# Optimization experiments

Measured on AMD Instinct MI355X. Metric: run time of the kernel, lower is better.

Reference implementation:

```python
import jax, jax.numpy as jnp
import numpy as np

B, H, V, L, M, D, C = 64, 512, 50000, 400, 128, 64, 64
HC = 2 * D + M + 4  # controller LSTM hidden size (one head)
EPS = 1e-8


def _lstm_step(x, h, c, Wih, Whh, bih, bhh):
    g = x @ Wih.T + bih + h @ Whh.T + bhh
    i, f, gg, o = jnp.split(g, 4, axis=-1)
    c2 = jax.nn.sigmoid(f) * c + jax.nn.sigmoid(i) * jnp.tanh(gg)
    return jax.nn.sigmoid(o) * jnp.tanh(c2), c2


def _head_params(hc):
    # slices exactly as in LSTMMemoryController (k=0, single head)
    keys = hc[:, :M]                               # [B, M]
    kstr = jnp.exp(hc[:, D:D + 1])                 # [B, 1]
    gate = jax.nn.sigmoid(hc[:, D + 1:D + 2])      # [B, 1]
    erase = jax.nn.sigmoid(hc[:, D + 4:M + D + 4]) # [B, M]
    add = jax.nn.sigmoid(hc[:, 2 * D + 4:M + 2 * D + 4])  # [B, M]
    return keys, kstr, gate, erase, add


def _addressing(keys, kstr, gate, heads, memory):
    # torch cosine_similarity(keys.unsqueeze(2), memory, dim=2):
    # keys [B,M] broadcast along memory_dim D
    num = keys * memory.sum(-1)                                   # [B, M]
    nk = jnp.maximum(jnp.abs(keys) * jnp.sqrt(jnp.float32(D)), EPS)
    nm = jnp.maximum(jnp.linalg.norm(memory, axis=-1), EPS)
    cos = num / (nk * nm)
    content = jax.nn.softmax(kstr * cos, axis=1)                  # [B, M]
    # faithful to original: heads[k] indexes axis 0 (k=0) -> shape [1, M]
    gated = gate * content + (1.0 - gate) * heads[0]
    return gated[:, None, :]                                      # [B, 1, M]


def reference(input_ids, h0, c0, encoder_outputs, word_occurrence_indicator,
              coverage, memory, read_heads, write_heads,
              read_h, read_c, write_h, write_c,
              emb, attn_W, attn_b, cov_W, state_W, comb_W, comb_b,
              rpre_W, rpre_b, wpre_W, wpre_b,
              r_Wih, r_Whh, r_bih, r_bhh,
              w_Wih, w_Whh, w_bih, w_bhh,
              l_Wih, l_Whh, l_bih, l_bhh,
              out_W, out_b):
    embedded = emb[input_ids]                                     # [B, H]
    ia = jnp.concatenate([embedded, h0], 1) @ attn_W.T + attn_b  # [B, L]
    tc = (coverage + ia) @ cov_W.T
    ts = c0 @ state_W.T
    aw = jax.nn.softmax(tc + ia + ts, axis=1)                     # [B, L]
    attn_applied = jnp.einsum('bl,blh->bh', aw, encoder_outputs)  # [B, H]
    out0 = jnp.concatenate([embedded, attn_applied], 1) @ comb_W.T + comb_b  # [B, H]

    hm = jnp.concatenate([h0, memory.reshape(-1, M * D)], 1)
    rh, rc = _lstm_step(hm @ rpre_W.T + rpre_b, read_h, read_c, r_Wih, r_Whh, r_bih, r_bhh)
    wh, wc = _lstm_step(hm @ wpre_W.T + wpre_b, write_h, write_c, w_Wih, w_Whh, w_bih, w_bhh)
    rk, rks, rg, _, _ = _head_params(rh)
    wk, wks, wg, we, wa = _head_params(wh)
    rw = _addressing(rk, rks, rg, read_heads, memory)             # [B, 1, M]
    ww = _addressing(wk, wks, wg, write_heads, memory)            # [B, 1, M]

    read_in = jnp.einsum('bkm,bmd->bkd', rw, memory).reshape(-1, D)
    h1, c1 = _lstm_step(jnp.concatenate([out0, read_in], 1), h0, c0,
                        l_Wih, l_Whh, l_bih, l_bhh)
    # residual (h1 + out0) is computed in the original but unused by its output path

    w0 = ww[:, 0, :, None]                                        # [B, M, 1]
    new_memory = memory * (1.0 - w0 * we[:, :, None]) + w0 * wa[:, :, None]
    new_coverage = coverage + ia

    log_probs = jax.nn.log_softmax(c1[:, None, :] @ out_W.T + out_b, axis=-1)  # [B, 1, V]
    return log_probs, h1, c1, new_memory, new_coverage


def setup_inputs() -> dict:
    key = jax.random.key(0)
    ks = iter(jax.random.split(key, 48))

    def rn(shape, fan_in):
        return jax.random.normal(next(ks), shape, jnp.float32) / np.sqrt(fan_in)

    inp = {
        'input_ids': jax.random.randint(next(ks), (B,), 0, V),
        'h0': jax.random.normal(next(ks), (B, H), jnp.float32),
        'c0': jax.random.normal(next(ks), (B, H), jnp.float32),
        'encoder_outputs': jax.random.normal(next(ks), (B, L, H), jnp.float32),
        'word_occurrence_indicator': jnp.zeros((B, L), jnp.float32),
        'coverage': jnp.zeros((B, L), jnp.float32),
        'memory': jax.random.normal(next(ks), (B, M, D), jnp.float32),
        'read_heads': jnp.zeros((B, 1, M), jnp.float32),
        'write_heads': jnp.zeros((B, 1, M), jnp.float32),
        'read_h': jnp.zeros((B, HC), jnp.float32),
        'read_c': jnp.zeros((B, HC), jnp.float32),
        'write_h': jnp.zeros((B, HC), jnp.float32),
        'write_c': jnp.zeros((B, HC), jnp.float32),
        'emb': rn((V, H), H),
        'attn_W': rn((L, 2 * H), 2 * H), 'attn_b': jnp.zeros((L,), jnp.float32),
        'cov_W': rn((L, L), L),
        'state_W': rn((L, H), H),
        'comb_W': rn((H, 2 * H), 2 * H), 'comb_b': jnp.zeros((H,), jnp.float32),
        'rpre_W': rn((C, M * D + H), M * D + H), 'rpre_b': jnp.zeros((C,), jnp.float32),
        'wpre_W': rn((C, M * D + H), M * D + H), 'wpre_b': jnp.zeros((C,), jnp.float32),
        'r_Wih': rn((4 * HC, C), C), 'r_Whh': rn((4 * HC, HC), HC),
        'r_bih': jnp.zeros((4 * HC,), jnp.float32), 'r_bhh': jnp.zeros((4 * HC,), jnp.float32),
        'w_Wih': rn((4 * HC, C), C), 'w_Whh': rn((4 * HC, HC), HC),
        'w_bih': jnp.zeros((4 * HC,), jnp.float32), 'w_bhh': jnp.zeros((4 * HC,), jnp.float32),
        'l_Wih': rn((4 * H, H + D), H + D), 'l_Whh': rn((4 * H, H), H),
        'l_bih': jnp.zeros((4 * H,), jnp.float32), 'l_bhh': jnp.zeros((4 * H,), jnp.float32),
        'out_W': rn((V, H), H), 'out_b': jnp.zeros((V,), jnp.float32),
    }
    return inp
```

## Files before the change

### kernel.cpp

```cpp
#include <hip/hip_runtime.h>
#include <math.h>

#define BB 64
#define HH 512
#define VV 50000
#define LL 400
#define MM 128
#define DD 64
#define HC 260
#define EPSF 1e-8f

typedef __attribute__((ext_vector_type(8))) short bf16x8;
typedef __attribute__((ext_vector_type(4))) float f32x4;
typedef __attribute__((address_space(1))) const void CGV;
typedef __attribute__((address_space(3))) void LV;

__device__ __forceinline__ float sigmoidf(float x){ return 1.0f/(1.0f+expf(-x)); }
__device__ __forceinline__ unsigned short bf16_rne(float f){
  unsigned u = __float_as_uint(f);
  return (unsigned short)((u + 0x7fffu + ((u >> 16) & 1u)) >> 16);
}
__device__ __forceinline__ float wave_max(float v){
  #pragma unroll
  for(int o=32;o;o>>=1) v = fmaxf(v, __shfl_xor(v,o));
  return v;
}
__device__ __forceinline__ float wave_sum(float v){
  #pragma unroll
  for(int o=32;o;o>>=1) v += __shfl_xor(v,o);
  return v;
}
__device__ __forceinline__ float dot4(float4 a, float4 w){
  return a.x*w.x + a.y*w.y + a.z*w.z + a.w*w.w;
}

__global__ __launch_bounds__(256) void k_ia_ts(const int* __restrict__ ids,
    const float* __restrict__ emb, const float* __restrict__ h0,
    const float* __restrict__ c0, const float* __restrict__ attn_W,
    const float* __restrict__ attn_b, const float* __restrict__ state_W,
    float* __restrict__ ia, float* __restrict__ ts){
  int b = blockIdx.y;
  int wid = threadIdx.x >> 6, lane = threadIdx.x & 63;
  if (blockIdx.x < 100){
    int n = blockIdx.x*4 + wid;
    const float4* E4 = (const float4*)(emb + (long)ids[b]*HH);
    const float4* H4 = (const float4*)(h0 + (long)b*HH);
    const float4* W4 = (const float4*)(attn_W + (long)n*1024);
    float acc = 0.f;
    #pragma unroll
    for (int i = 0; i < 4; i++){
      int k = lane + i*64;
      float4 a = (k < 128) ? E4[k] : H4[k-128];
      acc += dot4(a, W4[k]);
    }
    acc = wave_sum(acc);
    if (lane == 0) ia[b*LL + n] = acc + attn_b[n];
  } else {
    int n = (blockIdx.x-100)*4 + wid;
    const float4* A4 = (const float4*)(c0 + (long)b*HH);
    const float4* W4 = (const float4*)(state_W + (long)n*HH);
    float acc = 0.f;
    #pragma unroll
    for (int i = 0; i < 2; i++){
      int k = lane + i*64;
      acc += dot4(A4[k], W4[k]);
    }
    acc = wave_sum(acc);
    if (lane == 0) ts[b*LL + n] = acc;
  }
}

__global__ __launch_bounds__(256) void k_tc_cov(const float* __restrict__ cov,
    const float* __restrict__ ia, const float* __restrict__ cov_W,
    float* __restrict__ tc, float* __restrict__ ncov){
  int b = blockIdx.y;
  int wid = threadIdx.x >> 6, lane = threadIdx.x & 63;
  int n = blockIdx.x*4 + wid;
  const float4* C4 = (const float4*)(cov + (long)b*LL);
  const float4* I4 = (const float4*)(ia + (long)b*LL);
  const float4* W4 = (const float4*)(cov_W + (long)n*LL);
  float acc = 0.f;
  #pragma unroll
  for (int i = 0; i < 2; i++){
    int k = lane + i*64;
    if (k < 100){
      float4 a = C4[k], a2 = I4[k], w = W4[k];
      acc += (a.x+a2.x)*w.x + (a.y+a2.y)*w.y + (a.z+a2.z)*w.z + (a.w+a2.w)*w.w;
    }
  }
  acc = wave_sum(acc);
  if (lane == 0){
    tc[b*LL + n] = acc;
    ncov[b*LL + n] = cov[b*LL + n] + ia[b*LL + n];
  }
}

__global__ __launch_bounds__(256) void k_attn_part(const float* __restrict__ ia,
                                                   const float* __restrict__ ts,
                                                   const float* __restrict__ tc,
                                                   const float* __restrict__ enc,
                                                   float* __restrict__ part){
  int b = blockIdx.x, lc = blockIdx.y, t = threadIdx.x;
  __shared__ float sh[400];
  __shared__ float sm[4], ss[4];
  int i0 = t, i1 = t + 256;
  float x0 = ia[b*LL+i0] + ts[b*LL+i0] + tc[b*LL+i0];
  float x1 = (i1 < LL) ? (ia[b*LL+i1] + ts[b*LL+i1] + tc[b*LL+i1]) : -INFINITY;
  float m = wave_max(fmaxf(x0, x1));
  if ((t & 63) == 0) sm[t>>6] = m;
  __syncthreads();
  m = fmaxf(fmaxf(sm[0], sm[1]), fmaxf(sm[2], sm[3]));
  float e0 = expf(x0 - m);
  float e1 = (i1 < LL) ? expf(x1 - m) : 0.0f;
  sh[i0] = e0;
  if (i1 < LL) sh[i1] = e1;
  float s = wave_sum(e0 + e1);
  if ((t & 63) == 0) ss[t>>6] = s;
  __syncthreads();
  float inv = 1.0f / (ss[0] + ss[1] + ss[2] + ss[3]);
  const float* eb = enc + ((long)b*LL + lc*25)*HH;
  float a0 = 0.f, a1 = 0.f;
  for (int l = 0; l < 25; l++){
    float a = sh[lc*25 + l] * inv;
    a0 += a * eb[(long)l*HH + t];
    a1 += a * eb[(long)l*HH + t + 256];
  }
  part[((b*16 + lc) << 9) + t]       = a0;
  part[((b*16 + lc) << 9) + t + 256] = a1;
}

__global__ void k_attn_reduce(const float* __restrict__ part, float* __restrict__ attn){
  int idx = blockIdx.x*256 + threadIdx.x;
  if (idx >= BB*HH) return;
  int b = idx >> 9, h = idx & 511;
  float s = 0.f;
  #pragma unroll
  for (int lc = 0; lc < 16; lc++) s += part[((b*16 + lc) << 9) + h];
  attn[b*HH + h] = s;
}

__global__ __launch_bounds__(256) void k_comb(const int* __restrict__ ids,
    const float* __restrict__ emb, const float* __restrict__ attn,
    const float* __restrict__ comb_W, const float* __restrict__ comb_b,
    float* __restrict__ xcat3){
  int b = blockIdx.y;
  int wid = threadIdx.x >> 6, lane = threadIdx.x & 63;
  int n = blockIdx.x*4 + wid;
  const float4* E4 = (const float4*)(emb + (long)ids[b]*HH);
  const float4* A4 = (const float4*)(attn + (long)b*HH);
  const float4* W4 = (const float4*)(comb_W + (long)n*1024);
  float acc = 0.f;
  #pragma unroll
  for (int i = 0; i < 4; i++){
    int k = lane + i*64;
    float4 a = (k < 128) ? E4[k] : A4[k-128];
    acc += dot4(a, W4[k]);
  }
  acc = wave_sum(acc);
  if (lane == 0) xcat3[b*576 + n] = acc + comb_b[n];
}

__global__ __launch_bounds__(256) void k_pre(const float* __restrict__ h0,
    const float* __restrict__ mem, const float* __restrict__ rW,
    const float* __restrict__ wW, const float* __restrict__ rb,
    const float* __restrict__ wb, float* __restrict__ pre_r,
    float* __restrict__ pre_w){
  int wid = threadIdx.x >> 6, lane = threadIdx.x & 63;
  int n = blockIdx.x*4 + wid;
  int b = blockIdx.y;
  int which = blockIdx.z;
  const float* W = which ? wW : rW;
  const float4* W4 = (const float4*)(W + (long)n*8704);
  const float4* H4 = (const float4*)(h0 + (long)b*HH);
  const float4* M4 = (const float4*)(mem + (long)b*8192);
  float acc = 0.f;
  #pragma unroll 4
  for (int i = 0; i < 34; i++){
    int k = lane + i*64;
    float4 a = (k < 128) ? H4[k] : M4[k-128];
    acc += dot4(a, W4[k]);
  }
  acc = wave_sum(acc);
  if (lane == 0) (which ? pre_w : pre_r)[b*64 + n] = acc + (which ? wb : rb)[n];
}

__global__ __launch_bounds__(256) void k_gates(const float* __restrict__ pre_r,
    const float* __restrict__ pre_w, const float* __restrict__ read_h,
    const float* __restrict__ write_h, const float* __restrict__ read_c,
    const float* __restrict__ write_c,
    const float* __restrict__ rWih, const float* __restrict__ rWhh,
    const float* __restrict__ rbih, const float* __restrict__ rbhh,
    const float* __restrict__ wWih, const float* __restrict__ wWhh,
    const float* __restrict__ wbih, const float* __restrict__ wbhh,
    float* __restrict__ rh, float* __restrict__ wh){
  int which = blockIdx.z, b = blockIdx.y;
  int wid = threadIdx.x >> 6, lane = threadIdx.x & 63;
  int j = blockIdx.x*4 + wid;
  const float* pre = which ? pre_w : pre_r;
  const float* hhv = which ? write_h : read_h;
  const float* Wih = which ? wWih : rWih;
  const float* Whh = which ? wWhh : rWhh;
  float pv = pre[b*64 + lane];
  const float* hb = hhv + b*HC;
  float gv[4];
  #pragma unroll
  for (int g = 0; g < 4; g++){
    int n = g*HC + j;
    float acc = pv * Wih[n*64 + lane];
    const float* wr = Whh + (long)n*HC;
    #pragma unroll
    for (int i = 0; i < 5; i++){
      int k = lane + i*64;
      if (k < HC) acc += hb[k]*wr[k];
    }
    gv[g] = wave_sum(acc);
  }
  if (lane == 0){
    #pragma unroll
    for (int g = 0; g < 4; g++) gv[g] += (which ? wbih : rbih)[g*HC+j] + (which ? wbhh : rbhh)[g*HC+j];
    float c2 = sigmoidf(gv[1]) * (which ? write_c : read_c)[b*HC + j]
             + sigmoidf(gv[0]) * tanhf(gv[2]);
    (which ? wh : rh)[b*HC + j] = sigmoidf(gv[3]) * tanhf(c2);
  }
}

__global__ __launch_bounds__(128) void k_addr_mem(const float* __restrict__ rh,
                                                  const float* __restrict__ whv,
                                                  const float* __restrict__ rheads,
                                                  const float* __restrict__ wheads,
                                                  const float* __restrict__ mem,
                                                  float* __restrict__ xcat3,
                                                  float* __restrict__ nmem){
  int which = blockIdx.y;
  int b = blockIdx.x, m = threadIdx.x;
  const float* hc = which ? whv : rh;
  const float* heads0 = which ? wheads : rheads;
  const float* mr = mem + ((long)b*MM + m)*DD;
  float s = 0.f, q = 0.f;
  #pragma unroll 8
  for (int d = 0; d < DD; d++){ float v = mr[d]; s += v; q += v*v; }
  float key  = hc[b*HC + m];
  float kstr = expf(hc[b*HC + 64]);
  float gate = sigmoidf(hc[b*HC + 65]);
  float nk = fmaxf(fabsf(key)*8.0f, EPSF);
  float nm = fmaxf(sqrtf(q), EPSF);
  float z  = kstr * (key*s) / (nk*nm);
  __shared__ float sm[2], ss[2];
  __shared__ float wsh[128], weL[128], waL[128];
  float mx = wave_max(z);
  if ((m & 63) == 0) sm[m>>6] = mx;
  __syncthreads();
  mx = fmaxf(sm[0], sm[1]);
  float e = expf(z - mx);
  float w = wave_sum(e);
  if ((m & 63) == 0) ss[m>>6] = w;
  __syncthreads();
  float content = e / (ss[0] + ss[1]);
  float wv = gate*content + (1.0f - gate)*heads0[m];
  wsh[m] = wv;
  if (which){
    weL[m] = sigmoidf(whv[b*HC + 68 + m]);
    waL[m] = sigmoidf(whv[b*HC + 132 + m]);
  }
  __syncthreads();
  if (!which){
    if (m < DD){
      float acc = 0.f;
      #pragma unroll 8
      for (int mm = 0; mm < MM; mm++) acc += wsh[mm] * mem[((long)b*MM + mm)*DD + m];
      xcat3[b*576 + 512 + m] = acc;
    }
  } else {
    for (int idx = m; idx < MM*DD; idx += 128){
      int mm = idx >> 6;
      nmem[(long)b*8192 + idx] = mem[(long)b*8192 + idx]*(1.0f - wsh[mm]*weL[mm]) + wsh[mm]*waL[mm];
    }
  }
}

__global__ __launch_bounds__(256) void k_lstm_main(const float* __restrict__ xcat3,
                                                   const float* __restrict__ h0,
                                                   const float* __restrict__ lWih,
                                                   const float* __restrict__ lWhh,
                                                   const float* __restrict__ bih,
                                                   const float* __restrict__ bhh,
                                                   const float* __restrict__ c0,
                                                   float* __restrict__ h1,
                                                   float* __restrict__ c1,
                                                   unsigned short* __restrict__ c1b){
  int wid = threadIdx.x >> 6, lane = threadIdx.x & 63;
  int j = blockIdx.x*4 + wid;
  int b = blockIdx.y;
  const float4* A1 = (const float4*)(xcat3 + (long)b*576);
  const float4* A2 = (const float4*)(h0 + (long)b*HH);
  float gv[4];
  #pragma unroll
  for (int g = 0; g < 4; g++){
    int n = g*HH + j;
    const float4* W1 = (const float4*)(lWih + (long)n*576);
    const float4* W2 = (const float4*)(lWhh + (long)n*HH);
    float s = 0.f;
    #pragma unroll
    for (int i = 0; i < 3; i++){
      int k = lane + i*64;
      if (k < 144){ s += dot4(A1[k], W1[k]); }
    }
    #pragma unroll
    for (int i = 0; i < 2; i++){
      int k = lane + i*64;
      s += dot4(A2[k], W2[k]);
    }
    gv[g] = wave_sum(s);
  }
  if (lane == 0){
    #pragma unroll
    for (int g = 0; g < 4; g++){ int n = g*HH + j; gv[g] += bih[n] + bhh[n]; }
    float c2 = sigmoidf(gv[1])*c0[b*HH + j] + sigmoidf(gv[0])*tanhf(gv[2]);
    h1[b*HH + j] = sigmoidf(gv[3])*tanhf(c2);
    c1[b*HH + j] = c2;
    c1b[b*HH + j] = bf16_rne(c2);
  }
}

__global__ __launch_bounds__(128) void k_logits_mfma(const unsigned short* __restrict__ Ab,
                                                     const float* __restrict__ W,
                                                     const float* __restrict__ bias,
                                                     float* __restrict__ C){
  __shared__ float lds[16384];
  int wid = threadIdx.x >> 6, lane = threadIdx.x & 63;
  int strip = blockIdx.x*2 + wid;
  if (strip >= 3125) return;
  int nl = lane & 15;
  int q  = lane >> 4;
  int n  = strip*16 + nl;
  const float* Wlane = W + (long)n*HH + q*4;
  int base = wid*8192;

  #pragma unroll
  for (int ci = 0; ci < 32; ci++)
    __builtin_amdgcn_global_load_lds((CGV*)(Wlane + ci*16),
        (LV*)&lds[base + ci*256], 16, 0, 0);
  asm volatile("s_waitcnt vmcnt(0)" ::: "memory");
  __builtin_amdgcn_sched_barrier(0);

  const bf16x8* A0 = (const bf16x8*)Ab + (long)(0*16 + nl)*64 + q;
  const bf16x8* A1 = (const bf16x8*)Ab + (long)(1*16 + nl)*64 + q;
  const bf16x8* A2 = (const bf16x8*)Ab + (long)(2*16 + nl)*64 + q;
  const bf16x8* A3 = (const bf16x8*)Ab + (long)(3*16 + nl)*64 + q;
  f32x4 acc0 = {0.f,0.f,0.f,0.f}, acc1 = acc0, acc2 = acc0, acc3 = acc0;

  #pragma unroll
  for (int ks = 0; ks < 16; ks++){
    int off = base + (ks*2 + (q>>1))*256 + (q&1)*128 + nl*4;
    float4 w0 = *(const float4*)&lds[off];
    float4 w1 = *(const float4*)&lds[off + 64];
    bf16x8 bf;
    bf[0] = (short)bf16_rne(w0.x); bf[1] = (short)bf16_rne(w0.y);
    bf[2] = (short)bf16_rne(w0.z); bf[3] = (short)bf16_rne(w0.w);
    bf[4] = (short)bf16_rne(w1.x); bf[5] = (short)bf16_rne(w1.y);
    bf[6] = (short)bf16_rne(w1.z); bf[7] = (short)bf16_rne(w1.w);
    bf16x8 a0 = A0[ks*4];
    bf16x8 a1 = A1[ks*4];
    bf16x8 a2 = A2[ks*4];
    bf16x8 a3 = A3[ks*4];
    acc0 = __builtin_amdgcn_mfma_f32_16x16x32_bf16(a0, bf, acc0, 0, 0, 0);
    acc1 = __builtin_amdgcn_mfma_f32_16x16x32_bf16(a1, bf, acc1, 0, 0, 0);
    acc2 = __builtin_amdgcn_mfma_f32_16x16x32_bf16(a2, bf, acc2, 0, 0, 0);
    acc3 = __builtin_amdgcn_mfma_f32_16x16x32_bf16(a3, bf, acc3, 0, 0, 0);
  }
  float bv = bias[n];
  #pragma unroll
  for (int r = 0; r < 4; r++){
    int m = q*4 + r;
    C[(long)(m     )*VV + n] = acc0[r] + bv;
    C[(long)(m + 16)*VV + n] = acc1[r] + bv;
    C[(long)(m + 32)*VV + n] = acc2[r] + bv;
    C[(long)(m + 48)*VV + n] = acc3[r] + bv;
  }
}

__global__ __launch_bounds__(256) void k_ls1(const float* __restrict__ lp,
                                             float* __restrict__ pm, float* __restrict__ ps){
  int b = blockIdx.y, c = blockIdx.x, t = threadIdx.x;
  const float* row = lp + (long)b*VV + c*2000;
  float mx = -INFINITY;
  for (int i = t; i < 2000; i += 256) mx = fmaxf(mx, row[i]);
  __shared__ float sm[4], ss[4];
  mx = wave_max(mx);
  if ((t & 63) == 0) sm[t>>6] = mx;
  __syncthreads();
  mx = fmaxf(fmaxf(sm[0], sm[1]), fmaxf(sm[2], sm[3]));
  float s = 0.f;
  for (int i = t; i < 2000; i += 256) s += expf(row[i] - mx);
  s = wave_sum(s);
  if ((t & 63) == 0) ss[t>>6] = s;
  __syncthreads();
  if (t == 0){ pm[b*25 + c] = mx; ps[b*25 + c] = ss[0]+ss[1]+ss[2]+ss[3]; }
}

__global__ void k_ls2(const float* __restrict__ pm, const float* __restrict__ ps,
                      float* __restrict__ lse){
  int b = threadIdx.x;
  float m = -INFINITY;
  for (int c = 0; c < 25; c++) m = fmaxf(m, pm[b*25 + c]);
  float s = 0.f;
  for (int c = 0; c < 25; c++) s += ps[b*25 + c]*expf(pm[b*25 + c] - m);
  lse[b] = m + logf(s);
}

__global__ void k_ls3(float* __restrict__ lp, const float* __restrict__ lse){
  int idx = blockIdx.x*256 + threadIdx.x;
  if (idx >= BB*VV) return;
  int b = idx / VV;
  lp[idx] -= lse[b];
}

extern "C" void kernel_launch(void* const* d_in, const int* in_sizes, int n_in,
                              void* d_out, int out_size, void* d_ws, size_t ws_size,
                              hipStream_t stream) {
  const int*   ids     = (const int*)  d_in[0];
  const float* h0      = (const float*)d_in[1];
  const float* c0      = (const float*)d_in[2];
  const float* enc     = (const float*)d_in[3];
  const float* cov     = (const float*)d_in[5];
  const float* mem     = (const float*)d_in[6];
  const float* rheads  = (const float*)d_in[7];
  const float* wheads  = (const float*)d_in[8];
  const float* read_h  = (const float*)d_in[9];
  const float* read_c  = (const float*)d_in[10];
  const float* write_h = (const float*)d_in[11];
  const float* write_c = (const float*)d_in[12];
  const float* emb     = (const float*)d_in[13];
  const float* attn_W  = (const float*)d_in[14];
  const float* attn_b  = (const float*)d_in[15];
  const float* cov_W   = (const float*)d_in[16];
  const float* state_W = (const float*)d_in[17];
  const float* comb_W  = (const float*)d_in[18];
  const float* comb_b  = (const float*)d_in[19];
  const float* rpre_W  = (const float*)d_in[20];
  const float* rpre_b  = (const float*)d_in[21];
  const float* wpre_W  = (const float*)d_in[22];
  const float* wpre_b  = (const float*)d_in[23];
  const float* r_Wih   = (const float*)d_in[24];
  const float* r_Whh   = (const float*)d_in[25];
  const float* r_bih   = (const float*)d_in[26];
  const float* r_bhh   = (const float*)d_in[27];
  const float* w_Wih   = (const float*)d_in[28];
  const float* w_Whh   = (const float*)d_in[29];
  const float* w_bih   = (const float*)d_in[30];
  const float* w_bhh   = (const float*)d_in[31];
  const float* l_Wih   = (const float*)d_in[32];
  const float* l_Whh   = (const float*)d_in[33];
  const float* l_bih   = (const float*)d_in[34];
  const float* l_bhh   = (const float*)d_in[35];
  const float* out_W   = (const float*)d_in[36];
  const float* out_b   = (const float*)d_in[37];

  float* out  = (float*)d_out;
  float* lp   = out;
  float* h1   = out + 3200000;
  float* c1   = h1 + 32768;
  float* nmem = c1 + 32768;
  float* ncov = nmem + 524288;

  float* w = (float*)d_ws;
  float* xcat3 = w;
  float* ia    = xcat3 + 36864;
  float* ts    = ia + 25600;
  float* tc    = ts + 25600;
  float* attn  = tc + 25600;
  float* U     = attn + 32768;
  float* pre_r = U + 524288;
  float* pre_w = pre_r + 4096;
  float* rh    = pre_w + 4096;
  float* wh    = rh + 16640;
  float* pm    = wh + 16640;
  float* ps    = pm + 1600;
  float* lse   = ps + 1600;
  unsigned short* c1b = (unsigned short*)(lse + 64);

  k_ia_ts<<<dim3(200,64), 256, 0, stream>>>(ids, emb, h0, c0, attn_W, attn_b, state_W, ia, ts);
  k_tc_cov<<<dim3(100,64), 256, 0, stream>>>(cov, ia, cov_W, tc, ncov);
  k_attn_part<<<dim3(64,16), 256, 0, stream>>>(ia, ts, tc, enc, U);
  k_attn_reduce<<<128, 256, 0, stream>>>(U, attn);
  k_comb<<<dim3(128,64), 256, 0, stream>>>(ids, emb, attn, comb_W, comb_b, xcat3);

  k_pre<<<dim3(16,64,2), 256, 0, stream>>>(h0, mem, rpre_W, wpre_W, rpre_b, wpre_b, pre_r, pre_w);
  k_gates<<<dim3(65,64,2), 256, 0, stream>>>(pre_r, pre_w, read_h, write_h, read_c, write_c,
      r_Wih, r_Whh, r_bih, r_bhh, w_Wih, w_Whh, w_bih, w_bhh, rh, wh);
  k_addr_mem<<<dim3(64,2), 128, 0, stream>>>(rh, wh, rheads, wheads, mem, xcat3, nmem);

  k_lstm_main<<<dim3(128,64), 256, 0, stream>>>(xcat3, h0, l_Wih, l_Whh, l_bih, l_bhh,
                                                c0, h1, c1, c1b);

  k_logits_mfma<<<1563, 128, 0, stream>>>(c1b, out_W, out_b, lp);
  k_ls1<<<dim3(25,64), 256, 0, stream>>>(lp, pm, ps);
  k_ls2<<<1, 64, 0, stream>>>(pm, ps, lse);
  k_ls3<<<12500, 256, 0, stream>>>(lp, lse);
}
```

Baseline: 479.1 us.

## Restructure small GEMVs as batch-in-lanes kernels over transposed activations

Activations (embedding rows, h0, c0, memory, controller states) are packed into a batch-interleaved transposed layout, so each wavefront computes one output row for all 64 batch elements with lanes indexing batch. Each weight row is then read once and broadcast across the wave, where before it was re-read per batch element, and the per-output cross-lane reductions disappear. Several projection kernels are merged into two grouped launches, and a pack and an unpack kernel are added. The cost is extra transpose traffic, far fewer blocks (about 100 to 260) sharing the work, and long serial inner loops such as the 2048-step memory projection per wave.

Result: slower. 661.9 us (+38.1%).

```diff
diff --git a/kernel.cpp b/kernel.cpp
--- a/kernel.cpp
+++ b/kernel.cpp
@@ -30,82 +30,140 @@
   for(int o=32;o;o>>=1) v += __shfl_xor(v,o);
   return v;
 }
-__device__ __forceinline__ float dot4(float4 a, float4 w){
-  return a.x*w.x + a.y*w.y + a.z*w.z + a.w*w.w;
-}
-
-__global__ __launch_bounds__(256) void k_ia_ts(const int* __restrict__ ids,
+__device__ __forceinline__ float dot4(float4 w, float4 a){
+  return w.x*a.x + w.y*a.y + w.z*a.z + w.w*a.w;
+}
+
+
+__global__ __launch_bounds__(256) void k_pack(const int* __restrict__ ids,
     const float* __restrict__ emb, const float* __restrict__ h0,
-    const float* __restrict__ c0, const float* __restrict__ attn_W,
-    const float* __restrict__ attn_b, const float* __restrict__ state_W,
-    float* __restrict__ ia, float* __restrict__ ts){
-  int b = blockIdx.y;
-  int wid = threadIdx.x >> 6, lane = threadIdx.x & 63;
-  if (blockIdx.x < 100){
-    int n = blockIdx.x*4 + wid;
-    const float4* E4 = (const float4*)(emb + (long)ids[b]*HH);
-    const float4* H4 = (const float4*)(h0 + (long)b*HH);
-    const float4* W4 = (const float4*)(attn_W + (long)n*1024);
-    float acc = 0.f;
-    #pragma unroll
-    for (int i = 0; i < 4; i++){
-      int k = lane + i*64;
-      float4 a = (k < 128) ? E4[k] : H4[k-128];
-      acc += dot4(a, W4[k]);
-    }
-    acc = wave_sum(acc);
-    if (lane == 0) ia[b*LL + n] = acc + attn_b[n];
+    const float* __restrict__ c0, const float* __restrict__ read_h,
+    const float* __restrict__ write_h, const float* __restrict__ read_c,
+    const float* __restrict__ write_c, const float* __restrict__ mem,
+    float4* __restrict__ embT4, float4* __restrict__ h0T4, float4* __restrict__ c0T4,
+    float* __restrict__ c0Tp, float4* __restrict__ rhInT4, float4* __restrict__ whInT4,
+    float* __restrict__ rcT, float* __restrict__ wcT, float4* __restrict__ memT4){
+  int t = blockIdx.x*256 + threadIdx.x;
+  if (t < 8192){
+    int b = t & 63, kq = t >> 6;
+    float4 e = ((const float4*)emb)[(long)ids[b]*128 + kq];
+    float4 h = ((const float4*)h0)[b*128 + kq];
+    float4 c = ((const float4*)c0)[b*128 + kq];
+    embT4[t] = e; h0T4[t] = h; c0T4[t] = c;
+    c0Tp[(4*kq+0)*64+b] = c.x; c0Tp[(4*kq+1)*64+b] = c.y;
+    c0Tp[(4*kq+2)*64+b] = c.z; c0Tp[(4*kq+3)*64+b] = c.w;
+  } else if (t < 16512){
+    int s = t - 8192;
+    int which = s >= 4160; int u = which ? s-4160 : s;
+    int b = u & 63, kq = u >> 6;
+    float4 v = ((const float4*)(which ? write_h : read_h))[b*65 + kq];
+    (which ? whInT4 : rhInT4)[u] = v;
+  } else if (t < 49792){
+    int s = t - 16512;
+    int which = s >= 16640; int u = which ? s-16640 : s;
+    int b = u & 63, j = u >> 6;
+    (which ? wcT : rcT)[j*64+b] = (which ? write_c : read_c)[b*260 + j];
+  } else if (t < 180864){
+    int u = t - 49792;
+    int b = u & 63, kq = u >> 6;
+    memT4[u] = ((const float4*)mem)[b*2048 + kq];
+  }
+}
+
+__global__ __launch_bounds__(256) void k_blgA(const float4* __restrict__ embT4,
+    const float4* __restrict__ h0T4, const float4* __restrict__ c0T4,
+    const float4* __restrict__ memT4,
+    const float* __restrict__ attn_W, const float* __restrict__ attn_b,
+    const float* __restrict__ state_W,
+    const float* __restrict__ rpre_W, const float* __restrict__ wpre_W,
+    const float* __restrict__ rpre_b, const float* __restrict__ wpre_b,
+    float* __restrict__ iaT, float* __restrict__ tsT, float* __restrict__ preT){
+  int lane = threadIdx.x & 63;
+  int gw = __builtin_amdgcn_readfirstlane(blockIdx.x*4 + (threadIdx.x >> 6));
+  if (gw < 400){
+    int n = gw;
+    const float4* W4 = (const float4*)attn_W + (long)n*256;
+    float a0=0.f,a1=0.f,a2=0.f,a3=0.f;
+    #pragma unroll 8
+    for (int i = 0; i < 128; i++){
+      float4 a = embT4[i*64+lane]; float4 w = W4[i];
+      a0 += w.x*a.x; a1 += w.y*a.y; a2 += w.z*a.z; a3 += w.w*a.w;
+    }
+    #pragma unroll 8
+    for (int i = 0; i < 128; i++){
+      float4 a = h0T4[i*64+lane]; float4 w = W4[128+i];
+      a0 += w.x*a.x; a1 += w.y*a.y; a2 += w.z*a.z; a3 += w.w*a.w;
+    }
+    iaT[n*64+lane] = (a0+a1)+(a2+a3) + attn_b[n];
+  } else if (gw < 800){
+    int n = gw - 400;
+    const float4* W4 = (const float4*)state_W + (long)n*128;
+    float a0=0.f,a1=0.f,a2=0.f,a3=0.f;
+    #pragma unroll 8
+    for (int i = 0; i < 128; i++){
+      float4 a = c0T4[i*64+lane]; float4 w = W4[i];
+      a0 += w.x*a.x; a1 += w.y*a.y; a2 += w.z*a.z; a3 += w.w*a.w;
+    }
+    tsT[n*64+lane] = (a0+a1)+(a2+a3);
   } else {
-    int n = (blockIdx.x-100)*4 + wid;
-    const float4* A4 = (const float4*)(c0 + (long)b*HH);
-    const float4* W4 = (const float4*)(state_W + (long)n*HH);
-    float acc = 0.f;
-    #pragma unroll
-    for (int i = 0; i < 2; i++){
-      int k = lane + i*64;
-      acc += dot4(A4[k], W4[k]);
-    }
-    acc = wave_sum(acc);
-    if (lane == 0) ts[b*LL + n] = acc;
-  }
-}
-
-__global__ __launch_bounds__(256) void k_tc_cov(const float* __restrict__ cov,
-    const float* __restrict__ ia, const float* __restrict__ cov_W,
-    float* __restrict__ tc, float* __restrict__ ncov){
-  int b = blockIdx.y;
-  int wid = threadIdx.x >> 6, lane = threadIdx.x & 63;
-  int n = blockIdx.x*4 + wid;
-  const float4* C4 = (const float4*)(cov + (long)b*LL);
-  const float4* I4 = (const float4*)(ia + (long)b*LL);
-  const float4* W4 = (const float4*)(cov_W + (long)n*LL);
-  float acc = 0.f;
-  #pragma unroll
-  for (int i = 0; i < 2; i++){
-    int k = lane + i*64;
-    if (k < 100){
-      float4 a = C4[k], a2 = I4[k], w = W4[k];
-      acc += (a.x+a2.x)*w.x + (a.y+a2.y)*w.y + (a.z+a2.z)*w.z + (a.w+a2.w)*w.w;
-    }
-  }
-  acc = wave_sum(acc);
-  if (lane == 0){
-    tc[b*LL + n] = acc;
-    ncov[b*LL + n] = cov[b*LL + n] + ia[b*LL + n];
-  }
-}
-
-__global__ __launch_bounds__(256) void k_attn_part(const float* __restrict__ ia,
-                                                   const float* __restrict__ ts,
-                                                   const float* __restrict__ tc,
+    int r = gw - 800;
+    int which = r >> 6, n = r & 63;
+    const float4* W4 = (const float4*)(which ? wpre_W : rpre_W) + (long)n*2176;
+    float a0=0.f,a1=0.f,a2=0.f,a3=0.f;
+    #pragma unroll 8
+    for (int i = 0; i < 128; i++){
+      float4 a = h0T4[i*64+lane]; float4 w = W4[i];
+      a0 += w.x*a.x; a1 += w.y*a.y; a2 += w.z*a.z; a3 += w.w*a.w;
+    }
+    #pragma unroll 8
+    for (int i = 0; i < 2048; i++){
+      float4 a = memT4[i*64+lane]; float4 w = W4[128+i];
+      a0 += w.x*a.x; a1 += w.y*a.y; a2 += w.z*a.z; a3 += w.w*a.w;
+    }
+    preT[r*64+lane] = (a0+a1)+(a2+a3) + (which ? wpre_b : rpre_b)[n];
+  }
+}
+
+__global__ void k_covia(const float* __restrict__ cov, const float* __restrict__ iaT,
+                        float4* __restrict__ coviaT4, float4* __restrict__ ncov4){
+  int t = blockIdx.x*256 + threadIdx.x;
+  if (t >= 6400) return;
+  int b = t & 63, kq = t >> 6;
+  float4 c = ((const float4*)cov)[b*100 + kq];
+  float4 v;
+  v.x = c.x + iaT[(4*kq+0)*64+b];
+  v.y = c.y + iaT[(4*kq+1)*64+b];
+  v.z = c.z + iaT[(4*kq+2)*64+b];
+  v.w = c.w + iaT[(4*kq+3)*64+b];
+  coviaT4[kq*64+b] = v;
+  ncov4[b*100+kq] = v;
+}
+
+__global__ __launch_bounds__(256) void k_blg_tc(const float4* __restrict__ coviaT4,
+    const float* __restrict__ cov_W, float* __restrict__ tcT){
+  int lane = threadIdx.x & 63;
+  int n = __builtin_amdgcn_readfirstlane(blockIdx.x*4 + (threadIdx.x >> 6));
+  const float4* W4 = (const float4*)cov_W + (long)n*100;
+  float a0=0.f,a1=0.f,a2=0.f,a3=0.f;
+  #pragma unroll 4
+  for (int i = 0; i < 100; i++){
+    float4 a = coviaT4[i*64+lane]; float4 w = W4[i];
+    a0 += w.x*a.x; a1 += w.y*a.y; a2 += w.z*a.z; a3 += w.w*a.w;
+  }
+  tcT[n*64+lane] = (a0+a1)+(a2+a3);
+}
+
+__global__ __launch_bounds__(256) void k_attn_part(const float* __restrict__ iaT,
+                                                   const float* __restrict__ tsT,
+                                                   const float* __restrict__ tcT,
                                                    const float* __restrict__ enc,
                                                    float* __restrict__ part){
   int b = blockIdx.x, lc = blockIdx.y, t = threadIdx.x;
   __shared__ float sh[400];
   __shared__ float sm[4], ss[4];
   int i0 = t, i1 = t + 256;
-  float x0 = ia[b*LL+i0] + ts[b*LL+i0] + tc[b*LL+i0];
-  float x1 = (i1 < LL) ? (ia[b*LL+i1] + ts[b*LL+i1] + tc[b*LL+i1]) : -INFINITY;
+  float x0 = iaT[i0*64+b] + tsT[i0*64+b] + tcT[i0*64+b];
+  float x1 = (i1 < LL) ? (iaT[i1*64+b] + tsT[i1*64+b] + tcT[i1*64+b]) : -INFINITY;
   float m = wave_max(fmaxf(x0, x1));
   if ((t & 63) == 0) sm[t>>6] = m;
   __syncthreads();
@@ -129,119 +187,104 @@
   part[((b*16 + lc) << 9) + t + 256] = a1;
 }
 
-__global__ void k_attn_reduce(const float* __restrict__ part, float* __restrict__ attn){
-  int idx = blockIdx.x*256 + threadIdx.x;
-  if (idx >= BB*HH) return;
-  int b = idx >> 9, h = idx & 511;
-  float s = 0.f;
+__global__ void k_attn_reduce(const float4* __restrict__ part4, float4* __restrict__ attnT4){
+  int t = blockIdx.x*256 + threadIdx.x;
+  int b = t & 63, hq = t >> 6;
+  float4 s = {0.f,0.f,0.f,0.f};
   #pragma unroll
-  for (int lc = 0; lc < 16; lc++) s += part[((b*16 + lc) << 9) + h];
-  attn[b*HH + h] = s;
-}
-
-__global__ __launch_bounds__(256) void k_comb(const int* __restrict__ ids,
-    const float* __restrict__ emb, const float* __restrict__ attn,
-    const float* __restrict__ comb_W, const float* __restrict__ comb_b,
-    float* __restrict__ xcat3){
-  int b = blockIdx.y;
-  int wid = threadIdx.x >> 6, lane = threadIdx.x & 63;
-  int n = blockIdx.x*4 + wid;
-  const float4* E4 = (const float4*)(emb + (long)ids[b]*HH);
-  const float4* A4 = (const float4*)(attn + (long)b*HH);
-  const float4* W4 = (const float4*)(comb_W + (long)n*1024);
-  float acc = 0.f;
-  #pragma unroll
-  for (int i = 0; i < 4; i++){
-    int k = lane + i*64;
-    float4 a = (k < 128) ? E4[k] : A4[k-128];
-    acc += dot4(a, W4[k]);
-  }
-  acc = wave_sum(acc);
-  if (lane == 0) xcat3[b*576 + n] = acc + comb_b[n];
-}
-
-__global__ __launch_bounds__(256) void k_pre(const float* __restrict__ h0,
-    const float* __restrict__ mem, const float* __restrict__ rW,
-    const float* __restrict__ wW, const float* __restrict__ rb,
-    const float* __restrict__ wb, float* __restrict__ pre_r,
-    float* __restrict__ pre_w){
-  int wid = threadIdx.x >> 6, lane = threadIdx.x & 63;
-  int n = blockIdx.x*4 + wid;
-  int b = blockIdx.y;
-  int which = blockIdx.z;
-  const float* W = which ? wW : rW;
-  const float4* W4 = (const float4*)(W + (long)n*8704);
-  const float4* H4 = (const float4*)(h0 + (long)b*HH);
-  const float4* M4 = (const float4*)(mem + (long)b*8192);
-  float acc = 0.f;
-  #pragma unroll 4
-  for (int i = 0; i < 34; i++){
-    int k = lane + i*64;
-    float4 a = (k < 128) ? H4[k] : M4[k-128];
-    acc += dot4(a, W4[k]);
-  }
-  acc = wave_sum(acc);
-  if (lane == 0) (which ? pre_w : pre_r)[b*64 + n] = acc + (which ? wb : rb)[n];
-}
-
-__global__ __launch_bounds__(256) void k_gates(const float* __restrict__ pre_r,
-    const float* __restrict__ pre_w, const float* __restrict__ read_h,
-    const float* __restrict__ write_h, const float* __restrict__ read_c,
-    const float* __restrict__ write_c,
+  for (int lc = 0; lc < 16; lc++){
+    float4 p = part4[((b*16+lc)<<7) + hq];
+    s.x += p.x; s.y += p.y; s.z += p.z; s.w += p.w;
+  }
+  attnT4[hq*64 + b] = s;
+}
+
+__global__ __launch_bounds__(256) void k_blgB(const float4* __restrict__ embT4,
+    const float4* __restrict__ attnT4, const float* __restrict__ comb_W,
+    const float* __restrict__ comb_b, const float* __restrict__ preT,
+    const float4* __restrict__ rhInT4, const float4* __restrict__ whInT4,
+    const float* __restrict__ rcT, const float* __restrict__ wcT,
     const float* __restrict__ rWih, const float* __restrict__ rWhh,
     const float* __restrict__ rbih, const float* __restrict__ rbhh,
     const float* __restrict__ wWih, const float* __restrict__ wWhh,
     const float* __restrict__ wbih, const float* __restrict__ wbhh,
-    float* __restrict__ rh, float* __restrict__ wh){
-  int which = blockIdx.z, b = blockIdx.y;
-  int wid = threadIdx.x >> 6, lane = threadIdx.x & 63;
-  int j = blockIdx.x*4 + wid;
-  const float* pre = which ? pre_w : pre_r;
-  const float* hhv = which ? write_h : read_h;
-  const float* Wih = which ? wWih : rWih;
-  const float* Whh = which ? wWhh : rWhh;
-  float pv = pre[b*64 + lane];
-  const float* hb = hhv + b*HC;
-  float gv[4];
-  #pragma unroll
-  for (int g = 0; g < 4; g++){
-    int n = g*HC + j;
-    float acc = pv * Wih[n*64 + lane];
-    const float* wr = Whh + (long)n*HC;
-    #pragma unroll
-    for (int i = 0; i < 5; i++){
-      int k = lane + i*64;
-      if (k < HC) acc += hb[k]*wr[k];
-    }
-    gv[g] = wave_sum(acc);
-  }
-  if (lane == 0){
-    #pragma unroll
-    for (int g = 0; g < 4; g++) gv[g] += (which ? wbih : rbih)[g*HC+j] + (which ? wbhh : rbhh)[g*HC+j];
-    float c2 = sigmoidf(gv[1]) * (which ? write_c : read_c)[b*HC + j]
-             + sigmoidf(gv[0]) * tanhf(gv[2]);
-    (which ? wh : rh)[b*HC + j] = sigmoidf(gv[3]) * tanhf(c2);
-  }
-}
-
-__global__ __launch_bounds__(128) void k_addr_mem(const float* __restrict__ rh,
-                                                  const float* __restrict__ whv,
+    float* __restrict__ xc3T, float* __restrict__ rhT, float* __restrict__ whT){
+  int lane = threadIdx.x & 63;
+  int gw = __builtin_amdgcn_readfirstlane(blockIdx.x*4 + (threadIdx.x >> 6));
+  if (gw < 512){
+    int n = gw;
+    const float4* W4 = (const float4*)comb_W + (long)n*256;
+    float a0=0.f,a1=0.f,a2=0.f,a3=0.f;
+    #pragma unroll 8
+    for (int i = 0; i < 128; i++){
+      float4 a = embT4[i*64+lane]; float4 w = W4[i];
+      a0 += w.x*a.x; a1 += w.y*a.y; a2 += w.z*a.z; a3 += w.w*a.w;
+    }
+    #pragma unroll 8
+    for (int i = 0; i < 128; i++){
+      float4 a = attnT4[i*64+lane]; float4 w = W4[128+i];
+      a0 += w.x*a.x; a1 += w.y*a.y; a2 += w.z*a.z; a3 += w.w*a.w;
+    }
+    float v = (a0+a1)+(a2+a3) + comb_b[n];
+    xc3T[((n>>2)<<8) + (lane<<2) + (n&3)] = v;
+  } else {
+    int u = gw - 512;
+    int which = u >= 260;
+    int j = which ? u - 260 : u;
+    const float* Wih = which ? wWih : rWih;
+    const float* Whh = which ? wWhh : rWhh;
+    const float4* hT4 = which ? whInT4 : rhInT4;
+    float acc0=0.f, acc1=0.f, acc2=0.f, acc3=0.f;
+    #pragma unroll 4
+    for (int kq = 0; kq < 16; kq++){
+      float4 a;
+      a.x = preT[((which<<6)+4*kq+0)*64+lane];
+      a.y = preT[((which<<6)+4*kq+1)*64+lane];
+      a.z = preT[((which<<6)+4*kq+2)*64+lane];
+      a.w = preT[((which<<6)+4*kq+3)*64+lane];
+      acc0 += dot4(((const float4*)(Wih + (long)(0*HC+j)*64))[kq], a);
+      acc1 += dot4(((const float4*)(Wih + (long)(1*HC+j)*64))[kq], a);
+      acc2 += dot4(((const float4*)(Wih + (long)(2*HC+j)*64))[kq], a);
+      acc3 += dot4(((const float4*)(Wih + (long)(3*HC+j)*64))[kq], a);
+    }
+    #pragma unroll 4
+    for (int kq = 0; kq < 65; kq++){
+      float4 a = hT4[kq*64+lane];
+      acc0 += dot4(((const float4*)(Whh + (long)(0*HC+j)*HC))[kq], a);
+      acc1 += dot4(((const float4*)(Whh + (long)(1*HC+j)*HC))[kq], a);
+      acc2 += dot4(((const float4*)(Whh + (long)(2*HC+j)*HC))[kq], a);
+      acc3 += dot4(((const float4*)(Whh + (long)(3*HC+j)*HC))[kq], a);
+    }
+    const float* bih = which ? wbih : rbih;
+    const float* bhh = which ? wbhh : rbhh;
+    acc0 += bih[0*HC+j] + bhh[0*HC+j];
+    acc1 += bih[1*HC+j] + bhh[1*HC+j];
+    acc2 += bih[2*HC+j] + bhh[2*HC+j];
+    acc3 += bih[3*HC+j] + bhh[3*HC+j];
+    float cprev = (which ? wcT : rcT)[j*64+lane];
+    float c2 = sigmoidf(acc1)*cprev + sigmoidf(acc0)*tanhf(acc2);
+    (which ? whT : rhT)[j*64+lane] = sigmoidf(acc3)*tanhf(c2);
+  }
+}
+
+__global__ __launch_bounds__(128) void k_addr_mem(const float* __restrict__ rhT,
+                                                  const float* __restrict__ whT,
                                                   const float* __restrict__ rheads,
                                                   const float* __restrict__ wheads,
                                                   const float* __restrict__ mem,
-                                                  float* __restrict__ xcat3,
+                                                  float* __restrict__ xc3T,
                                                   float* __restrict__ nmem){
   int which = blockIdx.y;
   int b = blockIdx.x, m = threadIdx.x;
-  const float* hc = which ? whv : rh;
+  const float* hcT = which ? whT : rhT;
   const float* heads0 = which ? wheads : rheads;
   const float* mr = mem + ((long)b*MM + m)*DD;
   float s = 0.f, q = 0.f;
   #pragma unroll 8
   for (int d = 0; d < DD; d++){ float v = mr[d]; s += v; q += v*v; }
-  float key  = hc[b*HC + m];
-  float kstr = expf(hc[b*HC + 64]);
-  float gate = sigmoidf(hc[b*HC + 65]);
+  float key  = hcT[m*64 + b];
+  float kstr = expf(hcT[64*64 + b]);
+  float gate = sigmoidf(hcT[65*64 + b]);
   float nk = fmaxf(fabsf(key)*8.0f, EPSF);
   float nm = fmaxf(sqrtf(q), EPSF);
   float z  = kstr * (key*s) / (nk*nm);
@@ -259,8 +302,8 @@
   float wv = gate*content + (1.0f - gate)*heads0[m];
   wsh[m] = wv;
   if (which){
-    weL[m] = sigmoidf(whv[b*HC + 68 + m]);
-    waL[m] = sigmoidf(whv[b*HC + 132 + m]);
+    weL[m] = sigmoidf(whT[(68+m)*64 + b]);
+    waL[m] = sigmoidf(whT[(132+m)*64 + b]);
   }
   __syncthreads();
   if (!which){
@@ -268,7 +311,7 @@
       float acc = 0.f;
       #pragma unroll 8
       for (int mm = 0; mm < MM; mm++) acc += wsh[mm] * mem[((long)b*MM + mm)*DD + m];
-      xcat3[b*576 + 512 + m] = acc;
+      xc3T[((128 + (m>>2))<<8) + (b<<2) + (m&3)] = acc;
     }
   } else {
     for (int idx = m; idx < MM*DD; idx += 128){
@@ -278,48 +321,49 @@
   }
 }
 
-__global__ __launch_bounds__(256) void k_lstm_main(const float* __restrict__ xcat3,
-                                                   const float* __restrict__ h0,
-                                                   const float* __restrict__ lWih,
-                                                   const float* __restrict__ lWhh,
-                                                   const float* __restrict__ bih,
-                                                   const float* __restrict__ bhh,
-                                                   const float* __restrict__ c0,
-                                                   float* __restrict__ h1,
-                                                   float* __restrict__ c1,
-                                                   unsigned short* __restrict__ c1b){
-  int wid = threadIdx.x >> 6, lane = threadIdx.x & 63;
-  int j = blockIdx.x*4 + wid;
-  int b = blockIdx.y;
-  const float4* A1 = (const float4*)(xcat3 + (long)b*576);
-  const float4* A2 = (const float4*)(h0 + (long)b*HH);
-  float gv[4];
-  #pragma unroll
-  for (int g = 0; g < 4; g++){
-    int n = g*HH + j;
-    const float4* W1 = (const float4*)(lWih + (long)n*576);
-    const float4* W2 = (const float4*)(lWhh + (long)n*HH);
-    float s = 0.f;
-    #pragma unroll
-    for (int i = 0; i < 3; i++){
-      int k = lane + i*64;
-      if (k < 144){ s += dot4(A1[k], W1[k]); }
-    }
-    #pragma unroll
-    for (int i = 0; i < 2; i++){
-      int k = lane + i*64;
-      s += dot4(A2[k], W2[k]);
-    }
-    gv[g] = wave_sum(s);
-  }
-  if (lane == 0){
-    #pragma unroll
-    for (int g = 0; g < 4; g++){ int n = g*HH + j; gv[g] += bih[n] + bhh[n]; }
-    float c2 = sigmoidf(gv[1])*c0[b*HH + j] + sigmoidf(gv[0])*tanhf(gv[2]);
-    h1[b*HH + j] = sigmoidf(gv[3])*tanhf(c2);
-    c1[b*HH + j] = c2;
-    c1b[b*HH + j] = bf16_rne(c2);
-  }
+__global__ __launch_bounds__(256) void k_blg_lstm(const float4* __restrict__ xc3T4,
+    const float4* __restrict__ h0T4, const float* __restrict__ c0Tp,
+    const float* __restrict__ lWih, const float* __restrict__ lWhh,
+    const float* __restrict__ bih, const float* __restrict__ bhh,
+    float* __restrict__ h1T, float* __restrict__ c1T){
+  int lane = threadIdx.x & 63;
+  int j = __builtin_amdgcn_readfirstlane(blockIdx.x*4 + (threadIdx.x >> 6));
+  float acc0=0.f, acc1=0.f, acc2=0.f, acc3=0.f;
+  #pragma unroll 4
+  for (int kq = 0; kq < 144; kq++){
+    float4 a = xc3T4[kq*64+lane];
+    acc0 += dot4(((const float4*)(lWih + (long)(0*HH+j)*576))[kq], a);
+    acc1 += dot4(((const float4*)(lWih + (long)(1*HH+j)*576))[kq], a);
+    acc2 += dot4(((const float4*)(lWih + (long)(2*HH+j)*576))[kq], a);
+    acc3 += dot4(((const float4*)(lWih + (long)(3*HH+j)*576))[kq], a);
+  }
+  #pragma unroll 4
+  for (int kq = 0; kq < 128; kq++){
+    float4 a = h0T4[kq*64+lane];
+    acc0 += dot4(((const float4*)(lWhh + (long)(0*HH+j)*HH))[kq], a);
+    acc1 += dot4(((const float4*)(lWhh + (long)(1*HH+j)*HH))[kq], a);
+    acc2 += dot4(((const float4*)(lWhh + (long)(2*HH+j)*HH))[kq], a);
+    acc3 += dot4(((const float4*)(lWhh + (long)(3*HH+j)*HH))[kq], a);
+  }
+  acc0 += bih[0*HH+j] + bhh[0*HH+j];
+  acc1 += bih[1*HH+j] + bhh[1*HH+j];
+  acc2 += bih[2*HH+j] + bhh[2*HH+j];
+  acc3 += bih[3*HH+j] + bhh[3*HH+j];
+  float cprev = c0Tp[j*64+lane];
+  float c2 = sigmoidf(acc1)*cprev + sigmoidf(acc0)*tanhf(acc2);
+  h1T[j*64+lane] = sigmoidf(acc3)*tanhf(c2);
+  c1T[j*64+lane] = c2;
+}
+
+__global__ void k_unpack(const float* __restrict__ h1T, const float* __restrict__ c1T,
+                         float* __restrict__ h1, float* __restrict__ c1,
+                         unsigned short* __restrict__ c1b){
+  int t = blockIdx.x*256 + threadIdx.x;
+  int b = t >> 9, j = t & 511;
+  float c2 = c1T[j*64 + b];
+  h1[t] = h1T[j*64 + b];
+  c1[t] = c2;
+  c1b[t] = bf16_rne(c2);
 }
 
 __global__ __launch_bounds__(128) void k_logits_mfma(const unsigned short* __restrict__ Ab,
@@ -464,35 +508,49 @@
   float* ncov = nmem + 524288;
 
   float* w = (float*)d_ws;
-  float* xcat3 = w;
-  float* ia    = xcat3 + 36864;
-  float* ts    = ia + 25600;
-  float* tc    = ts + 25600;
-  float* attn  = tc + 25600;
-  float* U     = attn + 32768;
-  float* pre_r = U + 524288;
-  float* pre_w = pre_r + 4096;
-  float* rh    = pre_w + 4096;
-  float* wh    = rh + 16640;
-  float* pm    = wh + 16640;
-  float* ps    = pm + 1600;
-  float* lse   = ps + 1600;
+  float* embT4  = w;
+  float* h0T4   = embT4 + 32768;
+  float* c0T4   = h0T4 + 32768;
+  float* c0Tp   = c0T4 + 32768;
+  float* rhInT4 = c0Tp + 32768;
+  float* whInT4 = rhInT4 + 16640;
+  float* rcT    = whInT4 + 16640;
+  float* wcT    = rcT + 16640;
+  float* memT4  = wcT + 16640;
+  float* U      = memT4;
+  float* iaT    = memT4 + 524288;
+  float* tsT    = iaT + 25600;
+  float* tcT    = tsT + 25600;
+  float* coviaT = tcT + 25600;
+  float* attnT4 = coviaT + 25600;
+  float* xc3T   = attnT4 + 32768;
+  float* preT   = xc3T + 36864;
+  float* rhT    = preT + 8192;
+  float* whT    = rhT + 16640;
+  float* h1T    = whT + 16640;
+  float* c1T    = h1T + 32768;
+  float* pm     = c1T + 32768;
+  float* ps     = pm + 1600;
+  float* lse    = ps + 1600;
   unsigned short* c1b = (unsigned short*)(lse + 64);
 
-  k_ia_ts<<<dim3(200,64), 256, 0, stream>>>(ids, emb, h0, c0, attn_W, attn_b, state_W, ia, ts);
-  k_tc_cov<<<dim3(100,64), 256, 0, stream>>>(cov, ia, cov_W, tc, ncov);
-  k_attn_part<<<dim3(64,16), 256, 0, stream>>>(ia, ts, tc, enc, U);
-  k_attn_reduce<<<128, 256, 0, stream>>>(U, attn);
-  k_comb<<<dim3(128,64), 256, 0, stream>>>(ids, emb, attn, comb_W, comb_b, xcat3);
-
-  k_pre<<<dim3(16,64,2), 256, 0, stream>>>(h0, mem, rpre_W, wpre_W, rpre_b, wpre_b, pre_r, pre_w);
-  k_gates<<<dim3(65,64,2), 256, 0, stream>>>(pre_r, pre_w, read_h, write_h, read_c, write_c,
-      r_Wih, r_Whh, r_bih, r_bhh, w_Wih, w_Whh, w_bih, w_bhh, rh, wh);
-  k_addr_mem<<<dim3(64,2), 128, 0, stream>>>(rh, wh, rheads, wheads, mem, xcat3, nmem);
-
-  k_lstm_main<<<dim3(128,64), 256, 0, stream>>>(xcat3, h0, l_Wih, l_Whh, l_bih, l_bhh,
-                                                c0, h1, c1, c1b);
-
+  k_pack<<<707, 256, 0, stream>>>(ids, emb, h0, c0, read_h, write_h, read_c, write_c, mem,
+      (float4*)embT4, (float4*)h0T4, (float4*)c0T4, c0Tp,
+      (float4*)rhInT4, (float4*)whInT4, rcT, wcT, (float4*)memT4);
+  k_blgA<<<232, 256, 0, stream>>>((const float4*)embT4, (const float4*)h0T4,
+      (const float4*)c0T4, (const float4*)memT4, attn_W, attn_b, state_W,
+      rpre_W, wpre_W, rpre_b, wpre_b, iaT, tsT, preT);
+  k_covia<<<25, 256, 0, stream>>>(cov, iaT, (float4*)coviaT, (float4*)ncov);
+  k_blg_tc<<<100, 256, 0, stream>>>((const float4*)coviaT, cov_W, tcT);
+  k_attn_part<<<dim3(64,16), 256, 0, stream>>>(iaT, tsT, tcT, enc, U);
+  k_attn_reduce<<<32, 256, 0, stream>>>((const float4*)U, (float4*)attnT4);
+  k_blgB<<<258, 256, 0, stream>>>((const float4*)embT4, (const float4*)attnT4,
+      comb_W, comb_b, preT, (const float4*)rhInT4, (const float4*)whInT4, rcT, wcT,
+      r_Wih, r_Whh, r_bih, r_bhh, w_Wih, w_Whh, w_bih, w_bhh, xc3T, rhT, whT);
+  k_addr_mem<<<dim3(64,2), 128, 0, stream>>>(rhT, whT, rheads, wheads, mem, xc3T, nmem);
+  k_blg_lstm<<<128, 256, 0, stream>>>((const float4*)xc3T, (const float4*)h0T4, c0Tp,
+      l_Wih, l_Whh, l_bih, l_bhh, h1T, c1T);
+  k_unpack<<<128, 256, 0, stream>>>(h1T, c1T, h1, c1, c1b);
   k_logits_mfma<<<1563, 128, 0, stream>>>(c1b, out_W, out_b, lp);
   k_ls1<<<dim3(25,64), 256, 0, stream>>>(lp, pm, ps);
   k_ls2<<<1, 64, 0, stream>>>(pm, ps, lse);
```
